# Kernel optimization log

Measured on AMD Instinct MI355X. Metric: run time of the kernel, lower is better.

## Reference

```python
import jax, jax.numpy as jnp
import numpy as np

L, B, D, H, HD = 3, 16, 1024, 16, 64
T_PAST, S_ENC, FF, V = 1023, 1024, 4096, 20
SCALE = 1.0 / jnp.sqrt(jnp.float32(HD))
EPS = 1e-5


def setup_inputs() -> dict:
    key = jax.random.key(0)
    ks = jax.random.split(key, 32)
    w = 0.02
    inp = {
        'x': jax.random.normal(ks[0], (B, 1, D), jnp.float32),
        'enc': jax.random.normal(ks[1], (B, S_ENC, D), jnp.float32),
        'k_cache': jax.random.normal(ks[2], (L, B, H, T_PAST, HD), jnp.float32),
        'v_cache': jax.random.normal(ks[3], (L, B, H, T_PAST, HD), jnp.float32),
    }
    names = ['wq_s', 'wk_s', 'wv_s', 'wo_s', 'wq_c', 'wk_c', 'wv_c', 'wo_c']
    for i, n in enumerate(names):
        inp[n] = w * jax.random.normal(ks[4 + i], (L, D, D), jnp.float32)
        inp['b' + n[1:]] = w * jax.random.normal(ks[12 + i], (L, D), jnp.float32)
    inp['w1'] = w * jax.random.normal(ks[20], (L, D, FF), jnp.float32)
    inp['b1'] = w * jax.random.normal(ks[21], (L, FF), jnp.float32)
    inp['w2'] = w * jax.random.normal(ks[22], (L, FF, D), jnp.float32)
    inp['b2'] = w * jax.random.normal(ks[23], (L, D), jnp.float32)
    for j, n in enumerate(['ln1', 'ln2', 'ln3']):
        inp[n + '_g'] = jnp.ones((L, D), jnp.float32)
        inp[n + '_b'] = jnp.zeros((L, D), jnp.float32)
    inp['w_out'] = w * jax.random.normal(ks[24], (D, V), jnp.float32)
    inp['b_out'] = jnp.zeros((V,), jnp.float32)
    return inp


def _ln(x, g, b):
    m = jnp.mean(x, axis=-1, keepdims=True)
    v = jnp.mean(jnp.square(x - m), axis=-1, keepdims=True)
    return (x - m) * jax.lax.rsqrt(v + EPS) * g + b


def _heads(t):
    # [B, T, D] -> [B, H, T, HD]
    b, t_len, _ = t.shape
    return t.reshape(b, t_len, H, HD).transpose(0, 2, 1, 3)


def _mha(q_in, kv_in, wq, bq, wk, bk, wv, bv, wo, bo, past_k=None, past_v=None):
    Q = _heads(q_in @ wq + bq)            # [B,H,Lq,HD]
    K = _heads(kv_in @ wk + bk)           # [B,H,Lk,HD]
    Vv = _heads(kv_in @ wv + bv)
    if past_k is not None:
        K = jnp.concatenate([past_k, K], axis=2)   # cached append: [B,H,T+1,HD]
        Vv = jnp.concatenate([past_v, Vv], axis=2)
    scores = jnp.einsum('bhqd,bhkd->bhqk', Q, K) * SCALE
    attn = jax.nn.softmax(scores, axis=-1)
    out = jnp.einsum('bhqk,bhkd->bhqd', attn, Vv)  # [B,H,Lq,HD]
    b, _, lq, _ = out.shape
    out = out.transpose(0, 2, 1, 3).reshape(b, lq, D)
    return out @ wo + bo


def reference(x, enc, k_cache, v_cache, wq_s, bq_s, wk_s, bk_s, wv_s, bv_s,
              wo_s, bo_s, wq_c, bq_c, wk_c, bk_c, wv_c, bv_c, wo_c, bo_c,
              w1, b1, w2, b2, ln1_g, ln1_b, ln2_g, ln2_b, ln3_g, ln3_b,
              w_out, b_out):
    # One KV-cached decode step (query_len=1) through all decoder layers.
    for l in range(L):
        a = _mha(x, x, wq_s[l], bq_s[l], wk_s[l], bk_s[l], wv_s[l], bv_s[l],
                 wo_s[l], bo_s[l], past_k=k_cache[l], past_v=v_cache[l])
        x = _ln(x + a, ln1_g[l], ln1_b[l])
        c = _mha(x, enc, wq_c[l], bq_c[l], wk_c[l], bk_c[l], wv_c[l], bv_c[l],
                 wo_c[l], bo_c[l])
        x = _ln(x + c, ln2_g[l], ln2_b[l])
        f = jax.nn.relu(x @ w1[l] + b1[l]) @ w2[l] + b2[l]
        x = _ln(x + f, ln3_g[l], ln3_b[l])
    logits = x[:, 0, :] @ w_out + b_out   # [B, V]
    return logits
```

## Files before the change

### kernel.cpp

```cpp
#include <hip/hip_runtime.h>
#include <hip/hip_bf16.h>

#define NLAYER 3
#define BB 16
#define DD 1024
#define HH 16
#define HDIM 64
#define TPAST 1023
#define TTOT 1024
#define SENC 1024
#define FFD 4096
#define VOUT 20
#define ASCALE 0.125f
#define LNEPS 1e-5f

#define GLP(p) ((const __attribute__((address_space(1))) unsigned int*)(p))
#define LDP(p) ((__attribute__((address_space(3))) unsigned int*)(p))

typedef __attribute__((ext_vector_type(8))) short bf16x8;
typedef __attribute__((ext_vector_type(4))) float f32x4;

__device__ __forceinline__ float bf2f(unsigned short u) {
    union { unsigned int i; float f; } c; c.i = ((unsigned int)u) << 16; return c.f;
}
__device__ __forceinline__ unsigned short f2bf(float f) {
    union { float f; unsigned int i; } c; c.f = f;
    unsigned int x = c.i;
    unsigned int r = (x + 0x7fffu + ((x >> 16) & 1u)) >> 16;
    return (unsigned short)r;
}

__global__ __launch_bounds__(256) void cvt_bf16x4(
    const float* __restrict__ in, unsigned short* __restrict__ out, int n4) {
    int i = blockIdx.x * 256 + threadIdx.x;
    if (i < n4) {
        float4 v = ((const float4*)in)[i];
        ushort4 o;
        o.x = f2bf(v.x); o.y = f2bf(v.y); o.z = f2bf(v.z); o.w = f2bf(v.w);
        ((ushort4*)out)[i] = o;
    }
}

__global__ __launch_bounds__(256) void wt_bf16(
    const float* __restrict__ W, unsigned short* __restrict__ Wt) {
    __shared__ float ts[64][65];
    const int tid = threadIdx.x;
    const int k0 = blockIdx.y * 64, n0 = blockIdx.x * 64;
#pragma unroll
    for (int p = 0; p < 16; ++p) {
        int idx = p * 256 + tid;
        int r = idx >> 6, c = idx & 63;
        ts[r][c] = W[(size_t)(k0 + r) * DD + n0 + c];
    }
    __syncthreads();
#pragma unroll
    for (int p = 0; p < 16; ++p) {
        int idx = p * 256 + tid;
        int nn = idx >> 6, kk = idx & 63;
        Wt[(size_t)(n0 + nn) * DD + k0 + kk] = f2bf(ts[kk][nn]);
    }
}

__global__ __launch_bounds__(256) void gemm_mfma_bt(
    const unsigned short* __restrict__ A, const unsigned short* __restrict__ Bt,
    const float* __restrict__ bias, unsigned short* __restrict__ C) {
    const int K = DD, N = DD;
    __shared__ __align__(16) unsigned short As[128 * 32];
    __shared__ __align__(16) unsigned short Bs[128 * 32];
    const int tid = threadIdx.x;
    const int w = tid >> 6, l = tid & 63;
    const int m0 = blockIdx.y * 128, n0 = blockIdx.x * 128;
    const int wm = (w >> 1) * 64, wn = (w & 1) * 64;
    const int lm = l & 15, q = l >> 4;
    f32x4 acc[4][4] = {};

    const int c0 = w * 128 + l;
    const int c1 = c0 + 64;
    const unsigned short* Ag0 = A + (size_t)(m0 + (c0 >> 2)) * K + (c0 & 3) * 8;
    const unsigned short* Ag1 = A + (size_t)(m0 + (c1 >> 2)) * K + (c1 & 3) * 8;
    const unsigned short* Bg0 = Bt + (size_t)(n0 + (c0 >> 2)) * K + (c0 & 3) * 8;
    const unsigned short* Bg1 = Bt + (size_t)(n0 + (c1 >> 2)) * K + (c1 & 3) * 8;
    unsigned short* Asl0 = &As[w * 1024];
    unsigned short* Asl1 = &As[w * 1024 + 512];
    unsigned short* Bsl0 = &Bs[w * 1024];
    unsigned short* Bsl1 = &Bs[w * 1024 + 512];

    for (int k0 = 0; k0 < K; k0 += 32) {
        __builtin_amdgcn_global_load_lds(GLP(Ag0 + k0), LDP(Asl0), 16, 0, 0);
        __builtin_amdgcn_global_load_lds(GLP(Ag1 + k0), LDP(Asl1), 16, 0, 0);
        __builtin_amdgcn_global_load_lds(GLP(Bg0 + k0), LDP(Bsl0), 16, 0, 0);
        __builtin_amdgcn_global_load_lds(GLP(Bg1 + k0), LDP(Bsl1), 16, 0, 0);
        __syncthreads();
        const bf16x8* As8 = (const bf16x8*)As;
        const bf16x8* Bs8 = (const bf16x8*)Bs;
        bf16x8 af[4], bfr[4];
#pragma unroll
        for (int i = 0; i < 4; ++i) af[i] = As8[(wm + i * 16 + lm) * 4 + q];
#pragma unroll
        for (int j = 0; j < 4; ++j) bfr[j] = Bs8[(wn + j * 16 + lm) * 4 + q];
#pragma unroll
        for (int i = 0; i < 4; ++i)
#pragma unroll
            for (int j = 0; j < 4; ++j)
                acc[i][j] = __builtin_amdgcn_mfma_f32_16x16x32_bf16(
                    af[i], bfr[j], acc[i][j], 0, 0, 0);
        __syncthreads();
    }
#pragma unroll
    for (int j = 0; j < 4; ++j) {
        const int col = n0 + wn + j * 16 + lm;
        const float bj = bias[col];
#pragma unroll
        for (int i = 0; i < 4; ++i) {
            const int row = m0 + wm + i * 16 + q * 4;
#pragma unroll
            for (int r = 0; r < 4; ++r)
                C[(size_t)(row + r) * N + col] = f2bf(acc[i][j][r] + bj);
        }
    }
}

#define KSL 128
__global__ __launch_bounds__(64) void gemm16(
    const float* __restrict__ X, const float* __restrict__ W,
    float* __restrict__ Cacc, int K, int N) {
    __shared__ __align__(16) float xs[16][KSL];
    const int tid = threadIdx.x;
    const int n = blockIdx.x * 64 + tid;
    const int k0 = blockIdx.y * KSL;
    for (int idx = tid; idx < 16 * KSL; idx += 64) {
        int b = idx >> 7;
        int k = idx & (KSL - 1);
        xs[b][k] = X[(size_t)b * K + k0 + k];
    }
    __syncthreads();
    float acc[16] = {};
    for (int k = 0; k < KSL; k += 4) {
        const float* wp = W + (size_t)(k0 + k) * N + n;
        float w0 = wp[0], w1 = wp[N], w2 = wp[2 * (size_t)N], w3 = wp[3 * (size_t)N];
#pragma unroll
        for (int b = 0; b < 16; ++b) {
            float4 xv = *(const float4*)&xs[b][k];
            acc[b] = fmaf(xv.x, w0, fmaf(xv.y, w1, fmaf(xv.z, w2, fmaf(xv.w, w3, acc[b]))));
        }
    }
#pragma unroll
    for (int b = 0; b < 16; ++b)
        atomicAdd(&Cacc[(size_t)b * N + n], acc[b]);
}

__global__ __launch_bounds__(256) void attn_self(
    const float* __restrict__ q_raw, const float* __restrict__ bq,
    const float* __restrict__ kcache, const float* __restrict__ k_new,
    const float* __restrict__ bk,
    const float* __restrict__ vcache, const float* __restrict__ v_new,
    const float* __restrict__ bv, float* __restrict__ out) {
    const int h = blockIdx.x, b = blockIdx.y;
    const int tid = threadIdx.x;
    __shared__ __align__(16) float q[64];
    __shared__ float bks[64], bvs[64];
    __shared__ float sc[TTOT];
    __shared__ float red[256];
    if (tid < 64) {
        q[tid] = q_raw[b * DD + h * 64 + tid] + bq[h * 64 + tid];
        bks[tid] = bk[h * 64 + tid];
        bvs[tid] = bv[h * 64 + tid];
    }
    __syncthreads();
    const size_t bh = (size_t)(b * HH + h);
    for (int t = tid; t < TTOT; t += 256) {
        float dot = 0.f;
        if (t < TPAST) {
            const float4* kr = (const float4*)(kcache + (bh * TPAST + t) * HDIM);
            const float4* q4 = (const float4*)q;
#pragma unroll
            for (int i = 0; i < 16; ++i) {
                float4 kv = kr[i], qv = q4[i];
                dot += qv.x * kv.x + qv.y * kv.y + qv.z * kv.z + qv.w * kv.w;
            }
        } else {
            for (int i = 0; i < 64; ++i)
                dot += q[i] * (k_new[b * DD + h * 64 + i] + bks[i]);
        }
        sc[t] = dot * ASCALE;
    }
    __syncthreads();
    float lm = -1e30f;
    for (int t = tid; t < TTOT; t += 256) lm = fmaxf(lm, sc[t]);
    red[tid] = lm; __syncthreads();
    for (int s = 128; s > 0; s >>= 1) { if (tid < s) red[tid] = fmaxf(red[tid], red[tid + s]); __syncthreads(); }
    const float mx = red[0];
    __syncthreads();
    float ls = 0.f;
    for (int t = tid; t < TTOT; t += 256) { float p = __expf(sc[t] - mx); sc[t] = p; ls += p; }
    red[tid] = ls; __syncthreads();
    for (int s = 128; s > 0; s >>= 1) { if (tid < s) red[tid] += red[tid + s]; __syncthreads(); }
    const float inv = 1.0f / red[0];
    __syncthreads();
    const int hd = tid & 63, part = tid >> 6;
    float acc = 0.f;
    for (int t = part; t < TTOT; t += 4) {
        float v;
        if (t < TPAST) v = vcache[(bh * TPAST + t) * HDIM + hd];
        else           v = v_new[b * DD + h * 64 + hd] + bvs[hd];
        acc += sc[t] * v;
    }
    red[tid] = acc; __syncthreads();
    if (tid < 64)
        out[b * DD + h * 64 + tid] =
            (red[tid] + red[tid + 64] + red[tid + 128] + red[tid + 192]) * inv;
}

__global__ __launch_bounds__(256) void attn_cross(
    const float* __restrict__ q_raw, const float* __restrict__ bq,
    const unsigned short* __restrict__ Kc, const unsigned short* __restrict__ Vc,
    float* __restrict__ out) {
    const int h = blockIdx.x, b = blockIdx.y;
    const int tid = threadIdx.x;
    __shared__ __align__(16) float q[64];
    __shared__ float sc[SENC];
    __shared__ float red[256];
    if (tid < 64)
        q[tid] = q_raw[b * DD + h * 64 + tid] + bq[h * 64 + tid];
    __syncthreads();
    for (int s = tid; s < SENC; s += 256) {
        const uint4* kr = (const uint4*)(Kc + ((size_t)(b * SENC + s)) * DD + h * HDIM);
        float dot = 0.f;
#pragma unroll
        for (int i = 0; i < 8; ++i) {
            uint4 u = kr[i];
            dot += q[i * 8 + 0] * bf2f((unsigned short)u.x) + q[i * 8 + 1] * bf2f((unsigned short)(u.x >> 16));
            dot += q[i * 8 + 2] * bf2f((unsigned short)u.y) + q[i * 8 + 3] * bf2f((unsigned short)(u.y >> 16));
            dot += q[i * 8 + 4] * bf2f((unsigned short)u.z) + q[i * 8 + 5] * bf2f((unsigned short)(u.z >> 16));
            dot += q[i * 8 + 6] * bf2f((unsigned short)u.w) + q[i * 8 + 7] * bf2f((unsigned short)(u.w >> 16));
        }
        sc[s] = dot * ASCALE;
    }
    __syncthreads();
    float lm = -1e30f;
    for (int t = tid; t < SENC; t += 256) lm = fmaxf(lm, sc[t]);
    red[tid] = lm; __syncthreads();
    for (int s = 128; s > 0; s >>= 1) { if (tid < s) red[tid] = fmaxf(red[tid], red[tid + s]); __syncthreads(); }
    const float mx = red[0];
    __syncthreads();
    float ls = 0.f;
    for (int t = tid; t < SENC; t += 256) { float p = __expf(sc[t] - mx); sc[t] = p; ls += p; }
    red[tid] = ls; __syncthreads();
    for (int s = 128; s > 0; s >>= 1) { if (tid < s) red[tid] += red[tid + s]; __syncthreads(); }
    const float inv = 1.0f / red[0];
    __syncthreads();
    const int hd = tid & 63, part = tid >> 6;
    float acc = 0.f;
    for (int t = part; t < SENC; t += 4)
        acc += sc[t] * bf2f(Vc[((size_t)(b * SENC + t)) * DD + h * HDIM + hd]);
    red[tid] = acc; __syncthreads();
    if (tid < 64)
        out[b * DD + h * 64 + tid] =
            (red[tid] + red[tid + 64] + red[tid + 128] + red[tid + 192]) * inv;
}

__global__ __launch_bounds__(256) void ln_kernel(
    float* __restrict__ x, const float* __restrict__ a,
    const float* __restrict__ ab, const float* __restrict__ g,
    const float* __restrict__ bb) {
    const int b = blockIdx.x, tid = threadIdx.x;
    __shared__ float buf[DD];
    __shared__ float red[256];
    float ls = 0.f, lq = 0.f;
    for (int i = tid; i < DD; i += 256) {
        float v = x[b * DD + i] + a[b * DD + i] + ab[i];
        buf[i] = v; ls += v; lq += v * v;
    }
    red[tid] = ls; __syncthreads();
    for (int s = 128; s > 0; s >>= 1) { if (tid < s) red[tid] += red[tid + s]; __syncthreads(); }
    const float mean = red[0] * (1.0f / DD);
    __syncthreads();
    red[tid] = lq; __syncthreads();
    for (int s = 128; s > 0; s >>= 1) { if (tid < s) red[tid] += red[tid + s]; __syncthreads(); }
    const float var = red[0] * (1.0f / DD) - mean * mean;
    const float rstd = rsqrtf(var + LNEPS);
    for (int i = tid; i < DD; i += 256)
        x[b * DD + i] = (buf[i] - mean) * rstd * g[i] + bb[i];
}

__global__ __launch_bounds__(256) void relu_bias(
    const float* __restrict__ raw, const float* __restrict__ b1,
    float* __restrict__ out) {
    for (int i = blockIdx.x * 256 + threadIdx.x; i < BB * FFD; i += gridDim.x * 256)
        out[i] = fmaxf(0.f, raw[i] + b1[i & (FFD - 1)]);
}

__global__ __launch_bounds__(64) void logits_kernel(
    const float* __restrict__ x, const float* __restrict__ w_out,
    const float* __restrict__ b_out, float* __restrict__ out) {
    const int b = blockIdx.x / VOUT, v = blockIdx.x % VOUT;
    const int tid = threadIdx.x;
    float acc = 0.f;
    for (int k = tid; k < DD; k += 64)
        acc += x[b * DD + k] * w_out[(size_t)k * VOUT + v];
    for (int s = 32; s > 0; s >>= 1) acc += __shfl_down(acc, s);
    if (tid == 0) out[b * VOUT + v] = acc + b_out[v];
}

extern "C" void kernel_launch(void* const* d_in, const int* in_sizes, int n_in,
                              void* d_out, int out_size, void* d_ws, size_t ws_size,
                              hipStream_t stream) {
    const float* x_in    = (const float*)d_in[0];
    const float* enc     = (const float*)d_in[1];
    const float* k_cache = (const float*)d_in[2];
    const float* v_cache = (const float*)d_in[3];
    const float* wq_s = (const float*)d_in[4];  const float* bq_s = (const float*)d_in[5];
    const float* wk_s = (const float*)d_in[6];  const float* bk_s = (const float*)d_in[7];
    const float* wv_s = (const float*)d_in[8];  const float* bv_s = (const float*)d_in[9];
    const float* wo_s = (const float*)d_in[10]; const float* bo_s = (const float*)d_in[11];
    const float* wq_c = (const float*)d_in[12]; const float* bq_c = (const float*)d_in[13];
    const float* wk_c = (const float*)d_in[14]; const float* bk_c = (const float*)d_in[15];
    const float* wv_c = (const float*)d_in[16]; const float* bv_c = (const float*)d_in[17];
    const float* wo_c = (const float*)d_in[18]; const float* bo_c = (const float*)d_in[19];
    const float* w1 = (const float*)d_in[20];   const float* b1 = (const float*)d_in[21];
    const float* w2 = (const float*)d_in[22];   const float* b2 = (const float*)d_in[23];
    const float* ln1_g = (const float*)d_in[24]; const float* ln1_b = (const float*)d_in[25];
    const float* ln2_g = (const float*)d_in[26]; const float* ln2_b = (const float*)d_in[27];
    const float* ln3_g = (const float*)d_in[28]; const float* ln3_b = (const float*)d_in[29];
    const float* w_out = (const float*)d_in[30]; const float* b_out = (const float*)d_in[31];
    float* out = (float*)d_out;

    float* ws = (float*)d_ws;
    float* x_buf  = ws;
    float* mm_q   = ws + 16384;
    float* mm_k   = ws + 32768;
    float* mm_v   = ws + 49152;
    float* attn_o = ws + 65536;
    float* mm_p   = ws + 81920;
    float* mm_h1  = ws + 98304;
    float* h1a    = ws + 163840;
    unsigned short* Abf = (unsigned short*)(ws + 229376);
    unsigned short* Wkt = Abf + (size_t)BB * SENC * DD;
    unsigned short* Wvt = Wkt + (size_t)DD * DD;
    unsigned short* Kc  = Wvt + (size_t)DD * DD;
    unsigned short* Vc  = Kc + (size_t)BB * SENC * DD;

    hipMemcpyAsync(x_buf, x_in, (size_t)BB * DD * sizeof(float),
                   hipMemcpyDeviceToDevice, stream);

    cvt_bf16x4<<<(BB * SENC * DD / 4 + 255) / 256, 256, 0, stream>>>(
        enc, Abf, BB * SENC * DD / 4);

    const dim3 gBig(DD / 128, (BB * SENC) / 128);
    const dim3 gWt(16, 16);
    const dim3 gAttn(HH, BB);

    for (int l = 0; l < NLAYER; ++l) {
        const size_t oM = (size_t)l * DD * DD;
        const size_t oV = (size_t)l * DD;
        const size_t oC = (size_t)l * BB * HH * TPAST * HDIM;

        wt_bf16<<<gWt, 256, 0, stream>>>(wk_c + oM, Wkt);
        wt_bf16<<<gWt, 256, 0, stream>>>(wv_c + oM, Wvt);
        gemm_mfma_bt<<<gBig, 256, 0, stream>>>(Abf, Wkt, bk_c + oV, Kc);
        gemm_mfma_bt<<<gBig, 256, 0, stream>>>(Abf, Wvt, bv_c + oV, Vc);

        hipMemsetAsync(mm_q, 0, 3 * (size_t)BB * DD * sizeof(float), stream);
        gemm16<<<dim3(DD / 64, DD / KSL), 64, 0, stream>>>(x_buf, wq_s + oM, mm_q, DD, DD);
        gemm16<<<dim3(DD / 64, DD / KSL), 64, 0, stream>>>(x_buf, wk_s + oM, mm_k, DD, DD);
        gemm16<<<dim3(DD / 64, DD / KSL), 64, 0, stream>>>(x_buf, wv_s + oM, mm_v, DD, DD);
        attn_self<<<gAttn, 256, 0, stream>>>(mm_q, bq_s + oV, k_cache + oC, mm_k,
                                             bk_s + oV, v_cache + oC, mm_v, bv_s + oV,
                                             attn_o);
        hipMemsetAsync(mm_p, 0, (size_t)BB * DD * sizeof(float), stream);
        gemm16<<<dim3(DD / 64, DD / KSL), 64, 0, stream>>>(attn_o, wo_s + oM, mm_p, DD, DD);
        ln_kernel<<<BB, 256, 0, stream>>>(x_buf, mm_p, bo_s + oV, ln1_g + oV, ln1_b + oV);

        hipMemsetAsync(mm_q, 0, (size_t)BB * DD * sizeof(float), stream);
        gemm16<<<dim3(DD / 64, DD / KSL), 64, 0, stream>>>(x_buf, wq_c + oM, mm_q, DD, DD);
        attn_cross<<<gAttn, 256, 0, stream>>>(mm_q, bq_c + oV, Kc, Vc, attn_o);
        hipMemsetAsync(mm_p, 0, (size_t)BB * DD * sizeof(float), stream);
        gemm16<<<dim3(DD / 64, DD / KSL), 64, 0, stream>>>(attn_o, wo_c + oM, mm_p, DD, DD);
        ln_kernel<<<BB, 256, 0, stream>>>(x_buf, mm_p, bo_c + oV, ln2_g + oV, ln2_b + oV);

        hipMemsetAsync(mm_h1, 0, (size_t)BB * FFD * sizeof(float), stream);
        gemm16<<<dim3(FFD / 64, DD / KSL), 64, 0, stream>>>(x_buf, w1 + (size_t)l * DD * FFD,
                                                            mm_h1, DD, FFD);
        relu_bias<<<64, 256, 0, stream>>>(mm_h1, b1 + (size_t)l * FFD, h1a);
        hipMemsetAsync(mm_p, 0, (size_t)BB * DD * sizeof(float), stream);
        gemm16<<<dim3(DD / 64, FFD / KSL), 64, 0, stream>>>(h1a, w2 + (size_t)l * FFD * DD,
                                                            mm_p, FFD, DD);
        ln_kernel<<<BB, 256, 0, stream>>>(x_buf, mm_p, b2 + oV, ln3_g + oV, ln3_b + oV);
    }

    logits_kernel<<<BB * VOUT, 64, 0, stream>>>(x_buf, w_out, b_out, out);
}
```

Before: 2.269 ms.

## Reassociate cross-attention to skip encoder K/V projection and split self-attention over chunks

Cross-attention no longer projects the whole encoder output to K and V with bf16 MFMA GEMMs. Each (b,h) block instead folds the query through Wk (q·Wk^T), scores encoder rows directly, forms the probability-weighted encoder sum, and then applies Wv. The key bias is dropped because it shifts every score equally, and the value bias is added at the end. Self-attention over the KV cache is split into 8 sequence chunks that produce partial max/sum/accumulator values, followed by a combine kernel, which exposes more parallelism. This removes the two large per-layer GEMMs and the bf16 conversions, but each cross-attention block rereads 4 MB of fp32 encoder data and 256 blocks of 1024 threads may underuse memory bandwidth.

```diff
diff --git a/kernel.cpp b/kernel.cpp
--- a/kernel.cpp
+++ b/kernel.cpp
@@ -1,5 +1,4 @@
 #include <hip/hip_runtime.h>
-#include <hip/hip_bf16.h>
 
 #define NLAYER 3
 #define BB 16
@@ -13,112 +12,8 @@
 #define VOUT 20
 #define ASCALE 0.125f
 #define LNEPS 1e-5f
-
-#define GLP(p) ((const __attribute__((address_space(1))) unsigned int*)(p))
-#define LDP(p) ((__attribute__((address_space(3))) unsigned int*)(p))
-
-typedef __attribute__((ext_vector_type(8))) short bf16x8;
-typedef __attribute__((ext_vector_type(4))) float f32x4;
-
-__device__ __forceinline__ float bf2f(unsigned short u) {
-    union { unsigned int i; float f; } c; c.i = ((unsigned int)u) << 16; return c.f;
-}
-__device__ __forceinline__ unsigned short f2bf(float f) {
-    union { float f; unsigned int i; } c; c.f = f;
-    unsigned int x = c.i;
-    unsigned int r = (x + 0x7fffu + ((x >> 16) & 1u)) >> 16;
-    return (unsigned short)r;
-}
-
-__global__ __launch_bounds__(256) void cvt_bf16x4(
-    const float* __restrict__ in, unsigned short* __restrict__ out, int n4) {
-    int i = blockIdx.x * 256 + threadIdx.x;
-    if (i < n4) {
-        float4 v = ((const float4*)in)[i];
-        ushort4 o;
-        o.x = f2bf(v.x); o.y = f2bf(v.y); o.z = f2bf(v.z); o.w = f2bf(v.w);
-        ((ushort4*)out)[i] = o;
-    }
-}
-
-__global__ __launch_bounds__(256) void wt_bf16(
-    const float* __restrict__ W, unsigned short* __restrict__ Wt) {
-    __shared__ float ts[64][65];
-    const int tid = threadIdx.x;
-    const int k0 = blockIdx.y * 64, n0 = blockIdx.x * 64;
-#pragma unroll
-    for (int p = 0; p < 16; ++p) {
-        int idx = p * 256 + tid;
-        int r = idx >> 6, c = idx & 63;
-        ts[r][c] = W[(size_t)(k0 + r) * DD + n0 + c];
-    }
-    __syncthreads();
-#pragma unroll
-    for (int p = 0; p < 16; ++p) {
-        int idx = p * 256 + tid;
-        int nn = idx >> 6, kk = idx & 63;
-        Wt[(size_t)(n0 + nn) * DD + k0 + kk] = f2bf(ts[kk][nn]);
-    }
-}
-
-__global__ __launch_bounds__(256) void gemm_mfma_bt(
-    const unsigned short* __restrict__ A, const unsigned short* __restrict__ Bt,
-    const float* __restrict__ bias, unsigned short* __restrict__ C) {
-    const int K = DD, N = DD;
-    __shared__ __align__(16) unsigned short As[128 * 32];
-    __shared__ __align__(16) unsigned short Bs[128 * 32];
-    const int tid = threadIdx.x;
-    const int w = tid >> 6, l = tid & 63;
-    const int m0 = blockIdx.y * 128, n0 = blockIdx.x * 128;
-    const int wm = (w >> 1) * 64, wn = (w & 1) * 64;
-    const int lm = l & 15, q = l >> 4;
-    f32x4 acc[4][4] = {};
-
-    const int c0 = w * 128 + l;
-    const int c1 = c0 + 64;
-    const unsigned short* Ag0 = A + (size_t)(m0 + (c0 >> 2)) * K + (c0 & 3) * 8;
-    const unsigned short* Ag1 = A + (size_t)(m0 + (c1 >> 2)) * K + (c1 & 3) * 8;
-    const unsigned short* Bg0 = Bt + (size_t)(n0 + (c0 >> 2)) * K + (c0 & 3) * 8;
-    const unsigned short* Bg1 = Bt + (size_t)(n0 + (c1 >> 2)) * K + (c1 & 3) * 8;
-    unsigned short* Asl0 = &As[w * 1024];
-    unsigned short* Asl1 = &As[w * 1024 + 512];
-    unsigned short* Bsl0 = &Bs[w * 1024];
-    unsigned short* Bsl1 = &Bs[w * 1024 + 512];
-
-    for (int k0 = 0; k0 < K; k0 += 32) {
-        __builtin_amdgcn_global_load_lds(GLP(Ag0 + k0), LDP(Asl0), 16, 0, 0);
-        __builtin_amdgcn_global_load_lds(GLP(Ag1 + k0), LDP(Asl1), 16, 0, 0);
-        __builtin_amdgcn_global_load_lds(GLP(Bg0 + k0), LDP(Bsl0), 16, 0, 0);
-        __builtin_amdgcn_global_load_lds(GLP(Bg1 + k0), LDP(Bsl1), 16, 0, 0);
-        __syncthreads();
-        const bf16x8* As8 = (const bf16x8*)As;
-        const bf16x8* Bs8 = (const bf16x8*)Bs;
-        bf16x8 af[4], bfr[4];
-#pragma unroll
-        for (int i = 0; i < 4; ++i) af[i] = As8[(wm + i * 16 + lm) * 4 + q];
-#pragma unroll
-        for (int j = 0; j < 4; ++j) bfr[j] = Bs8[(wn + j * 16 + lm) * 4 + q];
-#pragma unroll
-        for (int i = 0; i < 4; ++i)
-#pragma unroll
-            for (int j = 0; j < 4; ++j)
-                acc[i][j] = __builtin_amdgcn_mfma_f32_16x16x32_bf16(
-                    af[i], bfr[j], acc[i][j], 0, 0, 0);
-        __syncthreads();
-    }
-#pragma unroll
-    for (int j = 0; j < 4; ++j) {
-        const int col = n0 + wn + j * 16 + lm;
-        const float bj = bias[col];
-#pragma unroll
-        for (int i = 0; i < 4; ++i) {
-            const int row = m0 + wm + i * 16 + q * 4;
-#pragma unroll
-            for (int r = 0; r < 4; ++r)
-                C[(size_t)(row + r) * N + col] = f2bf(acc[i][j][r] + bj);
-        }
-    }
-}
+#define NS 8
+#define CH 128
 
 #define KSL 128
 __global__ __launch_bounds__(64) void gemm16(
@@ -149,114 +44,166 @@
         atomicAdd(&Cacc[(size_t)b * N + n], acc[b]);
 }
 
-__global__ __launch_bounds__(256) void attn_self(
+__global__ __launch_bounds__(128) void attn_self_part(
     const float* __restrict__ q_raw, const float* __restrict__ bq,
     const float* __restrict__ kcache, const float* __restrict__ k_new,
     const float* __restrict__ bk,
     const float* __restrict__ vcache, const float* __restrict__ v_new,
-    const float* __restrict__ bv, float* __restrict__ out) {
-    const int h = blockIdx.x, b = blockIdx.y;
+    const float* __restrict__ bv, float* __restrict__ part) {
+    const int h = blockIdx.x, b = blockIdx.y, z = blockIdx.z;
     const int tid = threadIdx.x;
     __shared__ __align__(16) float q[64];
-    __shared__ float bks[64], bvs[64];
-    __shared__ float sc[TTOT];
-    __shared__ float red[256];
-    if (tid < 64) {
-        q[tid] = q_raw[b * DD + h * 64 + tid] + bq[h * 64 + tid];
-        bks[tid] = bk[h * 64 + tid];
-        bvs[tid] = bv[h * 64 + tid];
-    }
+    __shared__ float sc[CH];
+    __shared__ float red[128];
+    if (tid < 64) q[tid] = q_raw[b * DD + h * 64 + tid] + bq[h * 64 + tid];
     __syncthreads();
     const size_t bh = (size_t)(b * HH + h);
-    for (int t = tid; t < TTOT; t += 256) {
-        float dot = 0.f;
-        if (t < TPAST) {
-            const float4* kr = (const float4*)(kcache + (bh * TPAST + t) * HDIM);
-            const float4* q4 = (const float4*)q;
-#pragma unroll
-            for (int i = 0; i < 16; ++i) {
-                float4 kv = kr[i], qv = q4[i];
-                dot += qv.x * kv.x + qv.y * kv.y + qv.z * kv.z + qv.w * kv.w;
-            }
-        } else {
-            for (int i = 0; i < 64; ++i)
-                dot += q[i] * (k_new[b * DD + h * 64 + i] + bks[i]);
+    const int t = z * CH + tid;
+    float dot = 0.f;
+    if (t < TPAST) {
+        const float4* kr = (const float4*)(kcache + (bh * TPAST + t) * HDIM);
+        const float4* q4 = (const float4*)q;
+#pragma unroll
+        for (int i = 0; i < 16; ++i) {
+            float4 kv = kr[i], qv = q4[i];
+            dot += qv.x * kv.x + qv.y * kv.y + qv.z * kv.z + qv.w * kv.w;
         }
-        sc[t] = dot * ASCALE;
-    }
-    __syncthreads();
-    float lm = -1e30f;
-    for (int t = tid; t < TTOT; t += 256) lm = fmaxf(lm, sc[t]);
-    red[tid] = lm; __syncthreads();
-    for (int s = 128; s > 0; s >>= 1) { if (tid < s) red[tid] = fmaxf(red[tid], red[tid + s]); __syncthreads(); }
+    } else {
+        for (int i = 0; i < 64; ++i)
+            dot += q[i] * (k_new[b * DD + h * 64 + i] + bk[h * 64 + i]);
+    }
+    const float sval = dot * ASCALE;
+    red[tid] = sval;
+    __syncthreads();
+    for (int s = 64; s > 0; s >>= 1) {
+        if (tid < s) red[tid] = fmaxf(red[tid], red[tid + s]);
+        __syncthreads();
+    }
     const float mx = red[0];
     __syncthreads();
-    float ls = 0.f;
-    for (int t = tid; t < TTOT; t += 256) { float p = __expf(sc[t] - mx); sc[t] = p; ls += p; }
-    red[tid] = ls; __syncthreads();
-    for (int s = 128; s > 0; s >>= 1) { if (tid < s) red[tid] += red[tid + s]; __syncthreads(); }
-    const float inv = 1.0f / red[0];
-    __syncthreads();
-    const int hd = tid & 63, part = tid >> 6;
+    const float pv = __expf(sval - mx);
+    sc[tid] = pv;
+    red[tid] = pv;
+    __syncthreads();
+    for (int s = 64; s > 0; s >>= 1) {
+        if (tid < s) red[tid] += red[tid + s];
+        __syncthreads();
+    }
+    const float ssum = red[0];
+    __syncthreads();
+    const int hd = tid & 63, prt = tid >> 6;
     float acc = 0.f;
-    for (int t = part; t < TTOT; t += 4) {
+    for (int tl = prt; tl < CH; tl += 2) {
+        const int tg = z * CH + tl;
         float v;
-        if (t < TPAST) v = vcache[(bh * TPAST + t) * HDIM + hd];
-        else           v = v_new[b * DD + h * 64 + hd] + bvs[hd];
-        acc += sc[t] * v;
-    }
-    red[tid] = acc; __syncthreads();
-    if (tid < 64)
-        out[b * DD + h * 64 + tid] =
-            (red[tid] + red[tid + 64] + red[tid + 128] + red[tid + 192]) * inv;
-}
-
-__global__ __launch_bounds__(256) void attn_cross(
+        if (tg < TPAST) v = vcache[(bh * TPAST + tg) * HDIM + hd];
+        else            v = v_new[b * DD + h * 64 + hd] + bv[h * 64 + hd];
+        acc += sc[tl] * v;
+    }
+    red[tid] = acc;
+    __syncthreads();
+    float* pw = part + (bh * NS + z) * 66;
+    if (tid < 64) pw[2 + tid] = red[tid] + red[64 + tid];
+    if (tid == 0) { pw[0] = mx; pw[1] = ssum; }
+}
+
+__global__ __launch_bounds__(64) void attn_self_comb(
+    const float* __restrict__ part, float* __restrict__ out) {
+    const int bh = blockIdx.x;
+    const int tid = threadIdx.x;
+    float M = -1e30f;
+#pragma unroll
+    for (int z = 0; z < NS; ++z)
+        M = fmaxf(M, part[(size_t)(bh * NS + z) * 66]);
+    float S = 0.f, acc = 0.f;
+#pragma unroll
+    for (int z = 0; z < NS; ++z) {
+        const float* pz = part + (size_t)(bh * NS + z) * 66;
+        const float w = __expf(pz[0] - M);
+        S += pz[1] * w;
+        acc += pz[2 + tid] * w;
+    }
+    out[(size_t)bh * 64 + tid] = acc / S;
+}
+
+__global__ __launch_bounds__(1024) void cross_attn_lr(
     const float* __restrict__ q_raw, const float* __restrict__ bq,
-    const unsigned short* __restrict__ Kc, const unsigned short* __restrict__ Vc,
+    const float* __restrict__ Wk, const float* __restrict__ Wv,
+    const float* __restrict__ bv, const float* __restrict__ enc,
     float* __restrict__ out) {
     const int h = blockIdx.x, b = blockIdx.y;
     const int tid = threadIdx.x;
-    __shared__ __align__(16) float q[64];
-    __shared__ float sc[SENC];
-    __shared__ float red[256];
+    __shared__ __align__(16) float qs[64];
+    __shared__ __align__(16) float rks[DD];
+    __shared__ float p[SENC];
+    __shared__ float red[1024];
+    if (tid < 64) qs[tid] = q_raw[b * DD + h * 64 + tid] + bq[h * 64 + tid];
+    __syncthreads();
+    {
+        const float4* wr = (const float4*)(Wk + (size_t)tid * DD + h * 64);
+        const float4* q4 = (const float4*)qs;
+        float acc = 0.f;
+#pragma unroll
+        for (int i = 0; i < 16; ++i) {
+            float4 w = wr[i], q = q4[i];
+            acc += q.x * w.x + q.y * w.y + q.z * w.z + q.w * w.w;
+        }
+        rks[tid] = acc;
+    }
+    __syncthreads();
+    const float* eb = enc + (size_t)b * SENC * DD;
+    float sval;
+    {
+        const float4* er = (const float4*)(eb + (size_t)tid * DD);
+        const float4* r4 = (const float4*)rks;
+        float dot = 0.f;
+        for (int i = 0; i < 256; ++i) {
+            float4 e = er[i], r = r4[i];
+            dot += e.x * r.x + e.y * r.y + e.z * r.z + e.w * r.w;
+        }
+        sval = dot * ASCALE;
+        red[tid] = sval;
+    }
+    __syncthreads();
+    for (int s = 512; s > 0; s >>= 1) {
+        if (tid < s) red[tid] = fmaxf(red[tid], red[tid + s]);
+        __syncthreads();
+    }
+    const float mx = red[0];
+    __syncthreads();
+    const float pv = __expf(sval - mx);
+    p[tid] = pv;
+    red[tid] = pv;
+    __syncthreads();
+    for (int s = 512; s > 0; s >>= 1) {
+        if (tid < s) red[tid] += red[tid + s];
+        __syncthreads();
+    }
+    const float inv = 1.0f / red[0];
+    __syncthreads();
+    float cacc = 0.f;
+    for (int s = 0; s < SENC; s += 4) {
+        const float p0 = p[s], p1 = p[s + 1], p2 = p[s + 2], p3 = p[s + 3];
+        cacc += p0 * eb[(size_t)s * DD + tid];
+        cacc += p1 * eb[(size_t)(s + 1) * DD + tid];
+        cacc += p2 * eb[(size_t)(s + 2) * DD + tid];
+        cacc += p3 * eb[(size_t)(s + 3) * DD + tid];
+    }
+    __syncthreads();
+    rks[tid] = cacc * inv;
+    __syncthreads();
+    const int d = tid & 63, part = tid >> 6;
+    float oacc = 0.f;
+    for (int din = part; din < DD; din += 16)
+        oacc += rks[din] * Wv[(size_t)din * DD + h * 64 + d];
+    red[tid] = oacc;
+    __syncthreads();
+    for (int s = 512; s >= 64; s >>= 1) {
+        if (tid < s) red[tid] += red[tid + s];
+        __syncthreads();
+    }
     if (tid < 64)
-        q[tid] = q_raw[b * DD + h * 64 + tid] + bq[h * 64 + tid];
-    __syncthreads();
-    for (int s = tid; s < SENC; s += 256) {
-        const uint4* kr = (const uint4*)(Kc + ((size_t)(b * SENC + s)) * DD + h * HDIM);
-        float dot = 0.f;
-#pragma unroll
-        for (int i = 0; i < 8; ++i) {
-            uint4 u = kr[i];
-            dot += q[i * 8 + 0] * bf2f((unsigned short)u.x) + q[i * 8 + 1] * bf2f((unsigned short)(u.x >> 16));
-            dot += q[i * 8 + 2] * bf2f((unsigned short)u.y) + q[i * 8 + 3] * bf2f((unsigned short)(u.y >> 16));
-            dot += q[i * 8 + 4] * bf2f((unsigned short)u.z) + q[i * 8 + 5] * bf2f((unsigned short)(u.z >> 16));
-            dot += q[i * 8 + 6] * bf2f((unsigned short)u.w) + q[i * 8 + 7] * bf2f((unsigned short)(u.w >> 16));
-        }
-        sc[s] = dot * ASCALE;
-    }
-    __syncthreads();
-    float lm = -1e30f;
-    for (int t = tid; t < SENC; t += 256) lm = fmaxf(lm, sc[t]);
-    red[tid] = lm; __syncthreads();
-    for (int s = 128; s > 0; s >>= 1) { if (tid < s) red[tid] = fmaxf(red[tid], red[tid + s]); __syncthreads(); }
-    const float mx = red[0];
-    __syncthreads();
-    float ls = 0.f;
-    for (int t = tid; t < SENC; t += 256) { float p = __expf(sc[t] - mx); sc[t] = p; ls += p; }
-    red[tid] = ls; __syncthreads();
-    for (int s = 128; s > 0; s >>= 1) { if (tid < s) red[tid] += red[tid + s]; __syncthreads(); }
-    const float inv = 1.0f / red[0];
-    __syncthreads();
-    const int hd = tid & 63, part = tid >> 6;
-    float acc = 0.f;
-    for (int t = part; t < SENC; t += 4)
-        acc += sc[t] * bf2f(Vc[((size_t)(b * SENC + t)) * DD + h * HDIM + hd]);
-    red[tid] = acc; __syncthreads();
-    if (tid < 64)
-        out[b * DD + h * 64 + tid] =
-            (red[tid] + red[tid + 64] + red[tid + 128] + red[tid + 192]) * inv;
+        out[(size_t)b * DD + h * 64 + tid] = red[tid] + bv[h * 64 + tid];
 }
 
 __global__ __launch_bounds__(256) void ln_kernel(
@@ -324,56 +271,46 @@
     const float* ln3_g = (const float*)d_in[28]; const float* ln3_b = (const float*)d_in[29];
     const float* w_out = (const float*)d_in[30]; const float* b_out = (const float*)d_in[31];
     float* out = (float*)d_out;
+    (void)bk_c;
 
     float* ws = (float*)d_ws;
-    float* x_buf  = ws;
-    float* mm_q   = ws + 16384;
-    float* mm_k   = ws + 32768;
-    float* mm_v   = ws + 49152;
-    float* attn_o = ws + 65536;
-    float* mm_p   = ws + 81920;
-    float* mm_h1  = ws + 98304;
-    float* h1a    = ws + 163840;
-    unsigned short* Abf = (unsigned short*)(ws + 229376);
-    unsigned short* Wkt = Abf + (size_t)BB * SENC * DD;
-    unsigned short* Wvt = Wkt + (size_t)DD * DD;
-    unsigned short* Kc  = Wvt + (size_t)DD * DD;
-    unsigned short* Vc  = Kc + (size_t)BB * SENC * DD;
+    float* x_buf   = ws;
+    float* mm_q    = ws + 16384;
+    float* mm_k    = ws + 32768;
+    float* mm_v    = ws + 49152;
+    float* attn_o  = ws + 65536;
+    float* mm_p    = ws + 81920;
+    float* mm_h1   = ws + 98304;
+    float* h1a     = ws + 163840;
+    float* part_ws = ws + 229376;
 
     hipMemcpyAsync(x_buf, x_in, (size_t)BB * DD * sizeof(float),
                    hipMemcpyDeviceToDevice, stream);
 
-    cvt_bf16x4<<<(BB * SENC * DD / 4 + 255) / 256, 256, 0, stream>>>(
-        enc, Abf, BB * SENC * DD / 4);
-
-    const dim3 gBig(DD / 128, (BB * SENC) / 128);
-    const dim3 gWt(16, 16);
-    const dim3 gAttn(HH, BB);
+    const dim3 gAttnP(HH, BB, NS);
+    const dim3 gCross(HH, BB);
 
     for (int l = 0; l < NLAYER; ++l) {
         const size_t oM = (size_t)l * DD * DD;
         const size_t oV = (size_t)l * DD;
         const size_t oC = (size_t)l * BB * HH * TPAST * HDIM;
 
-        wt_bf16<<<gWt, 256, 0, stream>>>(wk_c + oM, Wkt);
-        wt_bf16<<<gWt, 256, 0, stream>>>(wv_c + oM, Wvt);
-        gemm_mfma_bt<<<gBig, 256, 0, stream>>>(Abf, Wkt, bk_c + oV, Kc);
-        gemm_mfma_bt<<<gBig, 256, 0, stream>>>(Abf, Wvt, bv_c + oV, Vc);
-
         hipMemsetAsync(mm_q, 0, 3 * (size_t)BB * DD * sizeof(float), stream);
         gemm16<<<dim3(DD / 64, DD / KSL), 64, 0, stream>>>(x_buf, wq_s + oM, mm_q, DD, DD);
         gemm16<<<dim3(DD / 64, DD / KSL), 64, 0, stream>>>(x_buf, wk_s + oM, mm_k, DD, DD);
         gemm16<<<dim3(DD / 64, DD / KSL), 64, 0, stream>>>(x_buf, wv_s + oM, mm_v, DD, DD);
-        attn_self<<<gAttn, 256, 0, stream>>>(mm_q, bq_s + oV, k_cache + oC, mm_k,
-                                             bk_s + oV, v_cache + oC, mm_v, bv_s + oV,
-                                             attn_o);
+        attn_self_part<<<gAttnP, 128, 0, stream>>>(mm_q, bq_s + oV, k_cache + oC, mm_k,
+                                                   bk_s + oV, v_cache + oC, mm_v, bv_s + oV,
+                                                   part_ws);
+        attn_self_comb<<<BB * HH, 64, 0, stream>>>(part_ws, attn_o);
         hipMemsetAsync(mm_p, 0, (size_t)BB * DD * sizeof(float), stream);
         gemm16<<<dim3(DD / 64, DD / KSL), 64, 0, stream>>>(attn_o, wo_s + oM, mm_p, DD, DD);
         ln_kernel<<<BB, 256, 0, stream>>>(x_buf, mm_p, bo_s + oV, ln1_g + oV, ln1_b + oV);
 
         hipMemsetAsync(mm_q, 0, (size_t)BB * DD * sizeof(float), stream);
         gemm16<<<dim3(DD / 64, DD / KSL), 64, 0, stream>>>(x_buf, wq_c + oM, mm_q, DD, DD);
-        attn_cross<<<gAttn, 256, 0, stream>>>(mm_q, bq_c + oV, Kc, Vc, attn_o);
+        cross_attn_lr<<<gCross, 1024, 0, stream>>>(mm_q, bq_c + oV, wk_c + oM, wv_c + oM,
+                                                   bv_c + oV, enc, attn_o);
         hipMemsetAsync(mm_p, 0, (size_t)BB * DD * sizeof(float), stream);
         gemm16<<<dim3(DD / 64, DD / KSL), 64, 0, stream>>>(attn_o, wo_c + oM, mm_p, DD, DD);
         ln_kernel<<<BB, 256, 0, stream>>>(x_buf, mm_p, bo_c + oV, ln2_g + oV, ln2_b + oV);
```

Measured after the change: 2.117 ms. 6.7% less time.
